# Kernel optimization log

Hardware: AMD Instinct MI355X
Metric: run time of the kernel (lower is better)

## Reference

```python
import jax, jax.numpy as jnp
import numpy as np

B, L1, L2, D = 128, 256, 256, 768
NEG = -10000.0
EPS = 1e-8


def setup_inputs() -> dict:
    key = jax.random.key(0)
    k1, k2, k3, k4 = jax.random.split(key, 4)
    v1 = jax.random.normal(k1, (B, L1, D), dtype=jnp.float32)
    v2 = jax.random.normal(k2, (B, L2, D), dtype=jnp.float32)
    # masks from random valid lengths in [L//2, L]
    len1 = jax.random.randint(k3, (B,), L1 // 2, L1 + 1)
    len2 = jax.random.randint(k4, (B,), L2 // 2, L2 + 1)
    mask1 = (jnp.arange(L1)[None, :] < len1[:, None]).astype(jnp.float32)
    mask2 = (jnp.arange(L2)[None, :] < len2[:, None]).astype(jnp.float32)
    return {"v1": v1, "mask1": mask1, "v2": v2, "mask2": mask2}


def reference(v1, mask1, v2, mask2):
    # alignment matrix [B, L1, L2]
    match = jnp.einsum('bld,bmd->blm', v1, v2)
    pair_mask = (mask1[:, :, None] * mask2[:, None, :]) > 0
    match = jnp.where(pair_mask, match, NEG)
    # attention over side 1: negative max-pool over L2, scaled
    s1 = -jnp.max(match, axis=2) / 100.0            # [B, L1]
    s1 = jnp.where(mask1 > 0, s1, NEG)
    attn1 = jax.nn.softmax(s1, axis=1)
    p1 = jnp.einsum('bld,bl->bd', v1, attn1)        # [B, D]
    # attention over side 2: negative max-pool over L1, scaled
    s2 = -jnp.max(match, axis=1) / 100.0            # [B, L2]
    s2 = jnp.where(mask2 > 0, s2, NEG)
    attn2 = jax.nn.softmax(s2, axis=1)
    p2 = jnp.einsum('bmd,bm->bd', v2, attn2)        # [B, D]
    # torch.nn.functional.cosine_similarity semantics (per-vector norm clamp)
    n1 = jnp.maximum(jnp.linalg.norm(p1, axis=-1), EPS)
    n2 = jnp.maximum(jnp.linalg.norm(p2, axis=-1), EPS)
    return jnp.sum(p1 * p2, axis=-1) / (n1 * n2)
```

## Files before the change

### kernel.cpp

```cpp
#include <hip/hip_runtime.h>


#define B_   128
#define L_   256
#define D_   768
#define NEGV (-10000.0f)
#define NEGU 0x39E3BFFFu

typedef _Float16 f16x8 __attribute__((ext_vector_type(8)));
typedef __fp16   h16x2 __attribute__((ext_vector_type(2)));
typedef float    f32x4 __attribute__((ext_vector_type(4)));

#define BT   128
#define BKF  64
#define NKT  (D_ / BKF)
#define LDH  72

__device__ __forceinline__ unsigned fmap(float f) {
    unsigned u = __float_as_uint(f);
    return (u & 0x80000000u) ? ~u : (u | 0x80000000u);
}
__device__ __forceinline__ float fdecode(unsigned u) {
    return __uint_as_float((u & 0x80000000u) ? (u ^ 0x80000000u) : ~u);
}
__device__ __forceinline__ float wred_max(float v) {
    #pragma unroll
    for (int o = 32; o; o >>= 1) v = fmaxf(v, __shfl_xor(v, o));
    return v;
}
__device__ __forceinline__ float wred_sum(float v) {
    #pragma unroll
    for (int o = 32; o; o >>= 1) v += __shfl_xor(v, o);
    return v;
}
__device__ __forceinline__ f16x8 cvt8(float4 a, float4 b) {
    union { h16x2 h2[4]; f16x8 h8; } u;
    u.h2[0] = __builtin_amdgcn_cvt_pkrtz(a.x, a.y);
    u.h2[1] = __builtin_amdgcn_cvt_pkrtz(a.z, a.w);
    u.h2[2] = __builtin_amdgcn_cvt_pkrtz(b.x, b.y);
    u.h2[3] = __builtin_amdgcn_cvt_pkrtz(b.z, b.w);
    return u.h8;
}

__global__ __launch_bounds__(512, 4)
void k_match(const float* __restrict__ v1, const float* __restrict__ m1,
             const float* __restrict__ v2, const float* __restrict__ m2,
             float* __restrict__ rmax_p, float* __restrict__ cmax_p)
{
    __shared__ __align__(16) _Float16 As[2][BT * LDH];
    __shared__ __align__(16) _Float16 Bs[2][BT * LDH];
    __shared__ unsigned rU[BT], cU[BT];
    __shared__ float m1s[BT], m2s[BT];
    __shared__ int sl1, sl2;

    const int bid = blockIdx.x;
    const int wg  = (bid & 7) * 64 + (bid >> 3);
    const int b = wg >> 2, ti = (wg >> 1) & 1, tj = wg & 1;

    const int t = threadIdx.x;
    const int lane = t & 63, w = t >> 6;
    const int wr = w >> 1, wc = w & 1;
    const int fr = lane & 15, fg = lane >> 4;

    if (t < BT) {
        rU[t] = NEGU; cU[t] = NEGU;
        m1s[t] = m1[b * L_ + ti * BT + t];
        m2s[t] = m2[b * L_ + tj * BT + t];
    }
    if (t == 0) { sl1 = 0; sl2 = 0; }
    __syncthreads();

    unsigned long long b1 = __ballot(t < BT && m1s[t] > 0.f);
    unsigned long long b2 = __ballot(t < BT && m2s[t] > 0.f);
    if (lane == 0 && b1) atomicAdd(&sl1, (int)__popcll(b1));
    if (lane == 0 && b2) atomicAdd(&sl2, (int)__popcll(b2));
    __syncthreads();
    const int len1b = sl1, len2b = sl2;

    f32x4 acc[2][4] = {};

    if (len1b > 0 && len2b > 0) {
        const int s_r = t >> 2, s_c = (t & 3) * 16;
        const bool pA = s_r < len1b;
        const bool pB = s_r < len2b;
        const float* ga = v1 + ((size_t)b * L_ + ti * BT + s_r) * D_ + s_c;
        const float* gb = v2 + ((size_t)b * L_ + tj * BT + s_r) * D_ + s_c;

        float4 ra[4], rb[4];

        #define GLOAD(kt) do {                                                    \
            const float* A_ = ga + (kt) * BKF;                                    \
            const float* C_ = gb + (kt) * BKF;                                    \
            if (pA) {                                                             \
                ra[0] = *(const float4*)(A_);      ra[1] = *(const float4*)(A_ + 4);  \
                ra[2] = *(const float4*)(A_ + 8);  ra[3] = *(const float4*)(A_ + 12); \
            }                                                                     \
            if (pB) {                                                             \
                rb[0] = *(const float4*)(C_);      rb[1] = *(const float4*)(C_ + 4);  \
                rb[2] = *(const float4*)(C_ + 8);  rb[3] = *(const float4*)(C_ + 12); \
            }                                                                     \
        } while (0)

        #define DSWRITE(buf) do {                                                 \
            if (pA) {                                                             \
                _Float16* da = &As[buf][s_r * LDH + s_c];                         \
                *(f16x8*)da       = cvt8(ra[0], ra[1]);                           \
                *(f16x8*)(da + 8) = cvt8(ra[2], ra[3]);                           \
            }                                                                     \
            if (pB) {                                                             \
                _Float16* db = &Bs[buf][s_r * LDH + s_c];                         \
                *(f16x8*)db       = cvt8(rb[0], rb[1]);                           \
                *(f16x8*)(db + 8) = cvt8(rb[2], rb[3]);                           \
            }                                                                     \
        } while (0)

        const bool vi0 = (wr * 32      ) < len1b;
        const bool vi1 = (wr * 32 + 16 ) < len1b;
        const bool vj0 = (wc * 64      ) < len2b;
        const bool vj1 = (wc * 64 + 16 ) < len2b;
        const bool vj2 = (wc * 64 + 32 ) < len2b;
        const bool vj3 = (wc * 64 + 48 ) < len2b;

        GLOAD(0);
        DSWRITE(0);
        __syncthreads();
        int cur = 0;
        for (int kt = 0; kt < NKT; ++kt) {
            if (kt + 1 < NKT) GLOAD(kt + 1);
            __builtin_amdgcn_sched_barrier(0);
            #pragma unroll
            for (int ks = 0; ks < 2; ++ks) {
                f16x8 af[2], bf[4];
                if (vi0) af[0] = *(const f16x8*)&As[cur][(wr * 32      + fr) * LDH + ks * 32 + fg * 8];
                if (vi1) af[1] = *(const f16x8*)&As[cur][(wr * 32 + 16 + fr) * LDH + ks * 32 + fg * 8];
                if (vj0) bf[0] = *(const f16x8*)&Bs[cur][(wc * 64      + fr) * LDH + ks * 32 + fg * 8];
                if (vj1) bf[1] = *(const f16x8*)&Bs[cur][(wc * 64 + 16 + fr) * LDH + ks * 32 + fg * 8];
                if (vj2) bf[2] = *(const f16x8*)&Bs[cur][(wc * 64 + 32 + fr) * LDH + ks * 32 + fg * 8];
                if (vj3) bf[3] = *(const f16x8*)&Bs[cur][(wc * 64 + 48 + fr) * LDH + ks * 32 + fg * 8];
                if (vi0) {
                    if (vj0) acc[0][0] = __builtin_amdgcn_mfma_f32_16x16x32_f16(af[0], bf[0], acc[0][0], 0, 0, 0);
                    if (vj1) acc[0][1] = __builtin_amdgcn_mfma_f32_16x16x32_f16(af[0], bf[1], acc[0][1], 0, 0, 0);
                    if (vj2) acc[0][2] = __builtin_amdgcn_mfma_f32_16x16x32_f16(af[0], bf[2], acc[0][2], 0, 0, 0);
                    if (vj3) acc[0][3] = __builtin_amdgcn_mfma_f32_16x16x32_f16(af[0], bf[3], acc[0][3], 0, 0, 0);
                }
                if (vi1) {
                    if (vj0) acc[1][0] = __builtin_amdgcn_mfma_f32_16x16x32_f16(af[1], bf[0], acc[1][0], 0, 0, 0);
                    if (vj1) acc[1][1] = __builtin_amdgcn_mfma_f32_16x16x32_f16(af[1], bf[1], acc[1][1], 0, 0, 0);
                    if (vj2) acc[1][2] = __builtin_amdgcn_mfma_f32_16x16x32_f16(af[1], bf[2], acc[1][2], 0, 0, 0);
                    if (vj3) acc[1][3] = __builtin_amdgcn_mfma_f32_16x16x32_f16(af[1], bf[3], acc[1][3], 0, 0, 0);
                }
            }
            __builtin_amdgcn_sched_barrier(0);
            if (kt + 1 < NKT) DSWRITE(cur ^ 1);
            __syncthreads();
            cur ^= 1;
        }
        #undef GLOAD
        #undef DSWRITE
    }

    #pragma unroll
    for (int i = 0; i < 2; ++i)
        #pragma unroll
        for (int r = 0; r < 4; ++r) {
            int row = wr * 32 + i * 16 + fg * 4 + r;
            bool rv = m1s[row] > 0.f;
            float mx = NEGV;
            #pragma unroll
            for (int j = 0; j < 4; ++j) {
                int col = wc * 64 + j * 16 + fr;
                float vv = (rv && m2s[col] > 0.f) ? acc[i][j][r] : NEGV;
                mx = fmaxf(mx, vv);
            }
            atomicMax(&rU[row], fmap(mx));
        }
    #pragma unroll
    for (int j = 0; j < 4; ++j) {
        int col = wc * 64 + j * 16 + fr;
        bool cv = m2s[col] > 0.f;
        float mx = NEGV;
        #pragma unroll
        for (int i = 0; i < 2; ++i)
            #pragma unroll
            for (int r = 0; r < 4; ++r) {
                int row = wr * 32 + i * 16 + fg * 4 + r;
                float vv = (cv && m1s[row] > 0.f) ? acc[i][j][r] : NEGV;
                mx = fmaxf(mx, vv);
            }
        atomicMax(&cU[col], fmap(mx));
    }
    __syncthreads();

    if (t < BT)
        rmax_p[((size_t)b * 2 + tj) * L_ + ti * BT + t] = fdecode(rU[t]);
    else if (t < 2 * BT)
        cmax_p[((size_t)b * 2 + ti) * L_ + tj * BT + (t - BT)] = fdecode(cU[t - BT]);
}

__global__ __launch_bounds__(512)
void k_attn_pool(const float* __restrict__ v1, const float* __restrict__ m1,
                 const float* __restrict__ v2, const float* __restrict__ m2,
                 const float* __restrict__ rmax_p, const float* __restrict__ cmax_p,
                 float* __restrict__ gpart)
{
    const int lin = (int)blockIdx.x;
    const int swz = (lin & 7) * 48 + (lin >> 3);
    const int b = swz / 3, chunk = swz % 3;

    const int t = threadIdx.x, lane = t & 63, w = t >> 6;
    const int h = t >> 8, l = t & 255;
    const int w4 = w & 3;

    __shared__ float attn[2][L_];
    __shared__ float sred[8];
    __shared__ int scnt[8];
    __shared__ __align__(16) float4 pbuf[2][4][64];
    __shared__ __align__(16) float4 pq[2][64];

    const float* mk = h ? m2 : m1;
    const float* P  = h ? cmax_p : rmax_p;

    float mkv = mk[b * L_ + l];
    float mxv = fmaxf(P[((size_t)b * 2 + 0) * L_ + l],
                      P[((size_t)b * 2 + 1) * L_ + l]);
    float s = (mkv > 0.f) ? (-mxv * 0.01f) : NEGV;

    unsigned long long bm = __ballot(mkv > 0.f);
    if (lane == 0) scnt[w] = (int)__popcll(bm);

    float wm = wred_max(s);
    if (lane == 0) sred[w] = wm;
    __syncthreads();
    float mx = fmaxf(fmaxf(sred[h * 4 + 0], sred[h * 4 + 1]),
                     fmaxf(sred[h * 4 + 2], sred[h * 4 + 3]));
    int nlen = scnt[h * 4 + 0] + scnt[h * 4 + 1] + scnt[h * 4 + 2] + scnt[h * 4 + 3];
    float e = expf(s - mx);
    __syncthreads();
    float ws = wred_sum(e);
    if (lane == 0) sred[w] = ws;
    __syncthreads();
    float sum = sred[h * 4 + 0] + sred[h * 4 + 1] + sred[h * 4 + 2] + sred[h * 4 + 3];
    attn[h][l] = e / sum;
    __syncthreads();

    const float* vb = (h ? v2 : v1) + (size_t)b * L_ * D_ + chunk * 256 + lane * 4;
    float4 p = {0.f, 0.f, 0.f, 0.f};
    #pragma unroll 4
    for (int ll = w4; ll < nlen; ll += 4) {
        float a = attn[h][ll];
        float4 x = *(const float4*)(vb + (size_t)ll * D_);
        p.x += a * x.x; p.y += a * x.y; p.z += a * x.z; p.w += a * x.w;
    }
    pbuf[h][w4][lane] = p;
    __syncthreads();
    if (w4 == 0) {
        float4 q0 = pbuf[h][0][lane], q1 = pbuf[h][1][lane];
        float4 q2 = pbuf[h][2][lane], q3 = pbuf[h][3][lane];
        float4 q = { q0.x + q1.x + q2.x + q3.x,
                     q0.y + q1.y + q2.y + q3.y,
                     q0.z + q1.z + q2.z + q3.z,
                     q0.w + q1.w + q2.w + q3.w };
        pq[h][lane] = q;
    }
    __syncthreads();

    if (t < 64) {
        float4 a = pq[0][lane], c = pq[1][lane];
        float dot = a.x * c.x + a.y * c.y + a.z * c.z + a.w * c.w;
        float n1  = a.x * a.x + a.y * a.y + a.z * a.z + a.w * a.w;
        float n2  = c.x * c.x + c.y * c.y + c.z * c.z + c.w * c.w;
        dot = wred_sum(dot); n1 = wred_sum(n1); n2 = wred_sum(n2);
        if (lane == 0) {
            float* gp = gpart + ((size_t)b * 3 + chunk) * 4;
            gp[0] = dot; gp[1] = n1; gp[2] = n2;
        }
    }
}

__global__ __launch_bounds__(128)
void k_cos(const float* __restrict__ gpart, float* __restrict__ out)
{
    const int b = threadIdx.x;
    const float* g = gpart + (size_t)b * 12;
    float dd = g[0] + g[4] + g[8];
    float aa = g[1] + g[5] + g[9];
    float cc = g[2] + g[6] + g[10];
    out[b] = dd / (fmaxf(sqrtf(aa), 1e-8f) * fmaxf(sqrtf(cc), 1e-8f));
}

extern "C" void kernel_launch(void* const* d_in, const int* in_sizes, int n_in,
                              void* d_out, int out_size, void* d_ws, size_t ws_size,
                              hipStream_t stream)
{
    const float* v1 = (const float*)d_in[0];
    const float* m1 = (const float*)d_in[1];
    const float* v2 = (const float*)d_in[2];
    const float* m2 = (const float*)d_in[3];
    float* out = (float*)d_out;

    float* rmax_p = (float*)d_ws;
    float* cmax_p = rmax_p + (size_t)B_ * 2 * L_;
    float* gpart  = cmax_p + (size_t)B_ * 2 * L_;

    k_match<<<dim3(4 * B_), 512, 0, stream>>>(v1, m1, v2, m2, rmax_p, cmax_p);

    k_attn_pool<<<dim3(B_ * 3), 512, 0, stream>>>(v1, m1, v2, m2, rmax_p, cmax_p, gpart);

    k_cos<<<dim3(1), 128, 0, stream>>>(gpart, out);
}
```

Baseline: 70.10 us.

## Load A operand fragments directly from global into registers, drop A LDS buffer

The v1 operand is no longer staged through shared memory. Each warp loads its own MFMA A-fragments from global memory as fp32, converts them to fp16 in registers, and feeds them straight to the MFMAs. This removes the A LDS writes and reads and halves shared memory per block, which may allow more blocks per CU. In exchange, A rows are loaded redundantly by both warp columns with less coalesced access, and the next tile's A load is issued late in the iteration, so its latency may be exposed.

Result: slower. 131.9 us (+88.1%).

```diff
diff --git a/kernel.cpp b/kernel.cpp
--- a/kernel.cpp
+++ b/kernel.cpp
@@ -47,7 +47,6 @@
              const float* __restrict__ v2, const float* __restrict__ m2,
              float* __restrict__ rmax_p, float* __restrict__ cmax_p)
 {
-    __shared__ __align__(16) _Float16 As[2][BT * LDH];
     __shared__ __align__(16) _Float16 Bs[2][BT * LDH];
     __shared__ unsigned rU[BT], cU[BT];
     __shared__ float m1s[BT], m2s[BT];
@@ -81,32 +80,41 @@
 
     if (len1b > 0 && len2b > 0) {
         const int s_r = t >> 2, s_c = (t & 3) * 16;
-        const bool pA = s_r < len1b;
         const bool pB = s_r < len2b;
-        const float* ga = v1 + ((size_t)b * L_ + ti * BT + s_r) * D_ + s_c;
         const float* gb = v2 + ((size_t)b * L_ + tj * BT + s_r) * D_ + s_c;
 
-        float4 ra[4], rb[4];
-
-        #define GLOAD(kt) do {                                                    \
-            const float* A_ = ga + (kt) * BKF;                                    \
+        const float* pa0 = v1 + ((size_t)b * L_ + ti * BT + wr * 32 +      fr) * D_ + fg * 8;
+        const float* pa1 = v1 + ((size_t)b * L_ + ti * BT + wr * 32 + 16 + fr) * D_ + fg * 8;
+
+        const bool vi0 = (wr * 32      ) < len1b;
+        const bool vi1 = (wr * 32 + 16 ) < len1b;
+        const bool vj0 = (wc * 64      ) < len2b;
+        const bool vj1 = (wc * 64 + 16 ) < len2b;
+        const bool vj2 = (wc * 64 + 32 ) < len2b;
+        const bool vj3 = (wc * 64 + 48 ) < len2b;
+
+        float4 rb[4];
+        float4 xa[2][2], ya[2][2];
+
+        #define GLOADB(kt) do {                                                   \
             const float* C_ = gb + (kt) * BKF;                                    \
-            if (pA) {                                                             \
-                ra[0] = *(const float4*)(A_);      ra[1] = *(const float4*)(A_ + 4);  \
-                ra[2] = *(const float4*)(A_ + 8);  ra[3] = *(const float4*)(A_ + 12); \
-            }                                                                     \
             if (pB) {                                                             \
                 rb[0] = *(const float4*)(C_);      rb[1] = *(const float4*)(C_ + 4);  \
                 rb[2] = *(const float4*)(C_ + 8);  rb[3] = *(const float4*)(C_ + 12); \
             }                                                                     \
         } while (0)
 
-        #define DSWRITE(buf) do {                                                 \
-            if (pA) {                                                             \
-                _Float16* da = &As[buf][s_r * LDH + s_c];                         \
-                *(f16x8*)da       = cvt8(ra[0], ra[1]);                           \
-                *(f16x8*)(da + 8) = cvt8(ra[2], ra[3]);                           \
+        #define GLOADA(kt) do {                                                   \
+            _Pragma("unroll")                                                     \
+            for (int ks = 0; ks < 2; ++ks) {                                      \
+                const float* A0 = pa0 + (kt) * BKF + ks * 32;                     \
+                const float* A1 = pa1 + (kt) * BKF + ks * 32;                     \
+                if (vi0) { xa[ks][0] = *(const float4*)A0; ya[ks][0] = *(const float4*)(A0 + 4); } \
+                if (vi1) { xa[ks][1] = *(const float4*)A1; ya[ks][1] = *(const float4*)(A1 + 4); } \
             }                                                                     \
+        } while (0)
+
+        #define DSWRITEB(buf) do {                                                \
             if (pB) {                                                             \
                 _Float16* db = &Bs[buf][s_r * LDH + s_c];                         \
                 *(f16x8*)db       = cvt8(rb[0], rb[1]);                           \
@@ -114,49 +122,51 @@
             }                                                                     \
         } while (0)
 
-        const bool vi0 = (wr * 32      ) < len1b;
-        const bool vi1 = (wr * 32 + 16 ) < len1b;
-        const bool vj0 = (wc * 64      ) < len2b;
-        const bool vj1 = (wc * 64 + 16 ) < len2b;
-        const bool vj2 = (wc * 64 + 32 ) < len2b;
-        const bool vj3 = (wc * 64 + 48 ) < len2b;
-
-        GLOAD(0);
-        DSWRITE(0);
+        GLOADA(0);
+        GLOADB(0);
+        DSWRITEB(0);
         __syncthreads();
         int cur = 0;
         for (int kt = 0; kt < NKT; ++kt) {
-            if (kt + 1 < NKT) GLOAD(kt + 1);
+            f16x8 afr[2][2];
+            #pragma unroll
+            for (int ks = 0; ks < 2; ++ks) {
+                if (vi0) afr[ks][0] = cvt8(xa[ks][0], ya[ks][0]);
+                if (vi1) afr[ks][1] = cvt8(xa[ks][1], ya[ks][1]);
+            }
+            if (kt + 1 < NKT) GLOADB(kt + 1);
             __builtin_amdgcn_sched_barrier(0);
             #pragma unroll
             for (int ks = 0; ks < 2; ++ks) {
-                f16x8 af[2], bf[4];
-                if (vi0) af[0] = *(const f16x8*)&As[cur][(wr * 32      + fr) * LDH + ks * 32 + fg * 8];
-                if (vi1) af[1] = *(const f16x8*)&As[cur][(wr * 32 + 16 + fr) * LDH + ks * 32 + fg * 8];
+                f16x8 bf[4];
                 if (vj0) bf[0] = *(const f16x8*)&Bs[cur][(wc * 64      + fr) * LDH + ks * 32 + fg * 8];
                 if (vj1) bf[1] = *(const f16x8*)&Bs[cur][(wc * 64 + 16 + fr) * LDH + ks * 32 + fg * 8];
                 if (vj2) bf[2] = *(const f16x8*)&Bs[cur][(wc * 64 + 32 + fr) * LDH + ks * 32 + fg * 8];
                 if (vj3) bf[3] = *(const f16x8*)&Bs[cur][(wc * 64 + 48 + fr) * LDH + ks * 32 + fg * 8];
                 if (vi0) {
-                    if (vj0) acc[0][0] = __builtin_amdgcn_mfma_f32_16x16x32_f16(af[0], bf[0], acc[0][0], 0, 0, 0);
-                    if (vj1) acc[0][1] = __builtin_amdgcn_mfma_f32_16x16x32_f16(af[0], bf[1], acc[0][1], 0, 0, 0);
-                    if (vj2) acc[0][2] = __builtin_amdgcn_mfma_f32_16x16x32_f16(af[0], bf[2], acc[0][2], 0, 0, 0);
-                    if (vj3) acc[0][3] = __builtin_amdgcn_mfma_f32_16x16x32_f16(af[0], bf[3], acc[0][3], 0, 0, 0);
+                    if (vj0) acc[0][0] = __builtin_amdgcn_mfma_f32_16x16x32_f16(afr[ks][0], bf[0], acc[0][0], 0, 0, 0);
+                    if (vj1) acc[0][1] = __builtin_amdgcn_mfma_f32_16x16x32_f16(afr[ks][0], bf[1], acc[0][1], 0, 0, 0);
+                    if (vj2) acc[0][2] = __builtin_amdgcn_mfma_f32_16x16x32_f16(afr[ks][0], bf[2], acc[0][2], 0, 0, 0);
+                    if (vj3) acc[0][3] = __builtin_amdgcn_mfma_f32_16x16x32_f16(afr[ks][0], bf[3], acc[0][3], 0, 0, 0);
                 }
                 if (vi1) {
-                    if (vj0) acc[1][0] = __builtin_amdgcn_mfma_f32_16x16x32_f16(af[1], bf[0], acc[1][0], 0, 0, 0);
-                    if (vj1) acc[1][1] = __builtin_amdgcn_mfma_f32_16x16x32_f16(af[1], bf[1], acc[1][1], 0, 0, 0);
-                    if (vj2) acc[1][2] = __builtin_amdgcn_mfma_f32_16x16x32_f16(af[1], bf[2], acc[1][2], 0, 0, 0);
-                    if (vj3) acc[1][3] = __builtin_amdgcn_mfma_f32_16x16x32_f16(af[1], bf[3], acc[1][3], 0, 0, 0);
+                    if (vj0) acc[1][0] = __builtin_amdgcn_mfma_f32_16x16x32_f16(afr[ks][1], bf[0], acc[1][0], 0, 0, 0);
+                    if (vj1) acc[1][1] = __builtin_amdgcn_mfma_f32_16x16x32_f16(afr[ks][1], bf[1], acc[1][1], 0, 0, 0);
+                    if (vj2) acc[1][2] = __builtin_amdgcn_mfma_f32_16x16x32_f16(afr[ks][1], bf[2], acc[1][2], 0, 0, 0);
+                    if (vj3) acc[1][3] = __builtin_amdgcn_mfma_f32_16x16x32_f16(afr[ks][1], bf[3], acc[1][3], 0, 0, 0);
                 }
             }
             __builtin_amdgcn_sched_barrier(0);
-            if (kt + 1 < NKT) DSWRITE(cur ^ 1);
+            if (kt + 1 < NKT) {
+                GLOADA(kt + 1);
+                DSWRITEB(cur ^ 1);
+            }
             __syncthreads();
             cur ^= 1;
         }
-        #undef GLOAD
-        #undef DSWRITE
+        #undef GLOADB
+        #undef GLOADA
+        #undef DSWRITEB
     }
 
     #pragma unroll
```
